# Kernel optimization log

Hardware: AMD Instinct MI355X
Metric: run time of the kernel (lower is better)

Reference implementation:

```python
import jax, jax.numpy as jnp
import numpy as np

B, S = 2, 256
CN, CE = 256, 128        # node / edge channels
A, H, V = 32, 8, 32      # attention_size, heads, value_size
AH, VH = A * H, V * H


def setup_inputs() -> dict:
    key = jax.random.key(0)
    ks = jax.random.split(key, 16)
    w = lambda k, shape: (jax.random.normal(k, shape) * 0.05).astype(jnp.float32)
    nodes = jax.random.normal(ks[0], (B, CN, S), dtype=jnp.float32)
    edges = jax.random.normal(ks[1], (B, CE, S, S), dtype=jnp.float32)
    lengths = jnp.array([S, (3 * S) // 4])            # padded-batch valid lengths
    mask = jnp.arange(S)[None, :] < lengths[:, None]  # (B, S) bool
    return dict(
        nodes=nodes, edges=edges, mask=mask,
        Wq=w(ks[2], (AH, CN)),
        Wk=w(ks[3], (AH, CN + CE)),
        Wv=w(ks[4], (VH, CN + CE)),
        Wo=w(ks[5], (CN, VH)),
        We=w(ks[6], (CE, VH + CE)),
        Wm1=w(ks[7], (CN, CN)), bm1=jnp.zeros((CN,), jnp.float32),
        Wm2=w(ks[8], (CN, CN)), bm2=jnp.zeros((CN,), jnp.float32),
        We1=w(ks[9], (CE, CE)), be1=jnp.zeros((CE,), jnp.float32),
        We2=w(ks[10], (CE, CE)), be2=jnp.zeros((CE,), jnp.float32),
        an0=(jax.random.normal(ks[11], (CN,)) * 0.1).astype(jnp.float32),
        an1=(jax.random.normal(ks[12], (CN,)) * 0.1).astype(jnp.float32),
        ae0=(jax.random.normal(ks[13], (CE,)) * 0.1).astype(jnp.float32),
        ae1=(jax.random.normal(ks[14], (CE,)) * 0.1).astype(jnp.float32),
    )


def _block(nodes, edges, mask, Wq, Wk, Wv, Wo, We,
           Wm1, bm1, Wm2, bm2, We1, be1, We2, be2, an0, an1, ae0, ae1):
    relu = jax.nn.relu
    b, _, s = nodes.shape
    # node MLP (1x1 conv, ReLU, 1x1 conv, ReLU) + ReZero residual; dropout in eval mode = identity
    h = relu(jnp.einsum('oc,bcs->bos', Wm1, nodes) + bm1[None, :, None])
    h = relu(jnp.einsum('oc,bcs->bos', Wm2, h) + bm2[None, :, None])
    nodes = nodes + an0[None, :, None] * h
    # edge MLP (1x1 conv2d) + ReZero residual
    g = relu(jnp.einsum('oc,bcij->boij', We1, edges) + be1[None, :, None, None])
    g = relu(jnp.einsum('oc,bcij->boij', We2, g) + be2[None, :, None, None])
    edges = edges + ae0[None, :, None, None] * g
    # materialized multi-head attention
    q = jnp.einsum('ac,bcs->bas', Wq, nodes).reshape(b, H, A, s)            # (B,H,A,S)
    ne = jnp.concatenate([jnp.broadcast_to(nodes[:, :, :, None], (b, CN, s, s)), edges], axis=1)
    k = jnp.einsum('ac,bcij->baij', Wk, ne).reshape(b, H, A, s, s)          # (B,H,A,S,S)
    v = jnp.einsum('vc,bcij->bvij', Wv, ne).reshape(b, H, V, s, s)          # (B,H,V,S,S)
    sim = jnp.einsum('bhai,bhaij->bhij', q, k) / jnp.sqrt(jnp.float32(A))   # (B,H,S,S)
    sim = jnp.where(mask[:, None, None, :], sim, jnp.float32(-1e9))
    sim = jax.nn.softmax(sim, axis=-1)
    mm = (mask[:, None, None, :] & mask[:, None, :, None]).astype(sim.dtype)  # (B,1,S,S)
    sim = sim * mm
    v = v * mm[:, None]
    nf = jnp.einsum('bhij,bhvij->bhvi', sim, v).reshape(b, H * V, s)        # (B,HV,S)
    node_att = jnp.einsum('oc,bcs->bos', Wo, nf)
    # edge features: broadcast node features along j, symmetrize via transpose+average
    ef = 0.5 * (nf[:, :, :, None] + nf[:, :, None, :])                      # (B,HV,S,S)
    edge_att = jnp.einsum('oc,bcij->boij', We, jnp.concatenate([ef, edges], axis=1))
    # ReZero residuals (project_* are Identity since in_size == out_size)
    nodes = nodes + an1[None, :, None] * node_att
    edges = edges + ae1[None, :, None, None] * edge_att
    # final masking
    nodes = nodes * mask[:, None, :].astype(nodes.dtype)
    edges = edges * mm
    return nodes, edges


def reference(nodes, edges, mask, Wq, Wk, Wv, Wo, We, Wm1, bm1, Wm2, bm2,
              We1, be1, We2, be2, an0, an1, ae0, ae1):
    return _block(nodes, edges, mask, Wq, Wk, Wv, Wo, We,
                  Wm1, bm1, Wm2, bm2, We1, be1, We2, be2, an0, an1, ae0, ae1)
```

## Files before the change

### kernel.cpp

```cpp
#include <hip/hip_runtime.h>
#include <hip/hip_bf16.h>
#include <cstdint>
#include <cstddef>

constexpr int B_  = 2;
constexpr int S_  = 256;
constexpr int CN_ = 256;
constexpr int CE_ = 128;
constexpr int A_  = 32;
constexpr int H_  = 8;
constexpr int V_  = 32;
constexpr int AH_ = A_ * H_;
constexpr int VH_ = V_ * H_;
constexpr int SS_ = S_ * S_;
constexpr int CNE_ = CN_ + CE_;

constexpr size_t OFF_N1   = 0;
constexpr size_t OFF_Q    = OFF_N1  + (size_t)B_*CN_*S_;
constexpr size_t OFF_VN   = OFF_Q   + (size_t)B_*AH_*S_;
constexpr size_t OFF_NF   = OFF_VN  + (size_t)B_*VH_*S_;
constexpr size_t OFF_WNF  = OFF_NF  + (size_t)B_*VH_*S_;
constexpr size_t OFF_WB1  = OFF_WNF + (size_t)B_*CE_*S_;
constexpr size_t OFF_WB2  = OFF_WB1 + 16384;
constexpr size_t OFF_WBE  = OFF_WB2 + 16384;
constexpr size_t OFF_WKT  = OFF_WBE + 16384;
constexpr size_t OFF_MASK = OFF_WKT + 32768;

__device__ inline uint16_t f2bf(float x) {
    uint32_t u = __float_as_uint(x);
    uint32_t r = (u + 0x7fffu + ((u >> 16) & 1u)) >> 16;
    return (uint16_t)r;
}
__device__ inline float bf2f(uint16_t h) {
    return __uint_as_float(((uint32_t)h) << 16);
}
__device__ inline uint32_t pack_split(float v) {
    uint32_t hi = (uint32_t)f2bf(v);
    float res = v - __uint_as_float(hi << 16);
    return (hi << 16) | (__float_as_uint(res) >> 16);
}
__device__ inline float unpack_f32(uint32_t p) {
    return __uint_as_float(p & 0xffff0000u) + __uint_as_float(p << 16);
}

typedef __attribute__((ext_vector_type(8))) short sh8;
typedef __attribute__((ext_vector_type(4))) short sh4;
typedef __attribute__((ext_vector_type(4))) float f32x4;

#define MFMA_B16(a, b, c) __builtin_amdgcn_mfma_f32_16x16x32_bf16((a), (b), (c), 0, 0, 0)

__device__ inline int eidx(int j, int c) {
    return (j * 136 + c) ^ (((j >> 3) & 7) << 3);
}

#define GEMM4_K256(WROW, XS, A0, A1, A2, A3)                                   \
    for (int c = 0; c < 256; c += 4) {                                         \
        float4 w  = *(const float4*)((WROW) + c);                              \
        float4 x0 = *(const float4*)((XS) + (c+0)*4);                          \
        float4 x1 = *(const float4*)((XS) + (c+1)*4);                          \
        float4 x2 = *(const float4*)((XS) + (c+2)*4);                          \
        float4 x3 = *(const float4*)((XS) + (c+3)*4);                          \
        A0 = fmaf(w.x,x0.x,fmaf(w.y,x1.x,fmaf(w.z,x2.x,fmaf(w.w,x3.x,A0))));   \
        A1 = fmaf(w.x,x0.y,fmaf(w.y,x1.y,fmaf(w.z,x2.y,fmaf(w.w,x3.y,A1))));   \
        A2 = fmaf(w.x,x0.z,fmaf(w.y,x1.z,fmaf(w.z,x2.z,fmaf(w.w,x3.z,A2))));   \
        A3 = fmaf(w.x,x0.w,fmaf(w.y,x1.w,fmaf(w.z,x2.w,fmaf(w.w,x3.w,A3))));   \
    }

__global__ void k_mask_norm(const unsigned char* __restrict__ mraw,
                            float* __restrict__ ws)
{
    int t = threadIdx.x;
    unsigned char b1 = mraw[1], b2 = mraw[2];
    float mv;
    if (b1 == (unsigned char)1) {
        mv = mraw[t] ? 1.f : 0.f;
    } else if (b2 == (unsigned char)128) {
        mv = (((const float*)mraw)[t] != 0.f) ? 1.f : 0.f;
    } else {
        mv = (((const int*)mraw)[t] != 0) ? 1.f : 0.f;
    }
    ws[OFF_MASK + t] = mv;
}

__global__ void k_wprep(const float* __restrict__ We1_,
                        const float* __restrict__ We2_,
                        const float* __restrict__ We_,
                        const float* __restrict__ Wk_,
                        float* __restrict__ ws)
{
    int idx = blockIdx.x * 256 + threadIdx.x;
    int m = idx >> 14;
    if (m < 3) {
        int r = idx & 16383;
        int o = r >> 7, c = r & 127;
        ushort* wb1 = (ushort*)(ws + OFF_WB1);
        ushort* wb2 = (ushort*)(ws + OFF_WB2);
        ushort* wbe = (ushort*)(ws + OFF_WBE);
        if (m == 0)      wb1[r] = f2bf(We1_[o*CE_ + c]);
        else if (m == 1) wb2[r] = f2bf(We2_[o*CE_ + c]);
        else             wbe[r] = f2bf(We_[o*CNE_ + CN_ + c]);
    } else {
        int r = idx - 49152;
        int a = r >> 10, h = (r >> 7) & 7, c = r & 127;
        ws[OFF_WKT + r] = Wk_[(size_t)(h*A_ + a)*CNE_ + CN_ + c];
    }
}

__global__ __launch_bounds__(256)
void k_node_mlp_qv(const float* __restrict__ nodes,
                   const float* __restrict__ Wm1, const float* __restrict__ bm1,
                   const float* __restrict__ Wm2, const float* __restrict__ bm2,
                   const float* __restrict__ an0,
                   const float* __restrict__ Wq,  const float* __restrict__ Wv,
                   float* __restrict__ ws)
{
    __shared__ float xs[CN_ * 4];
    __shared__ float hs[CN_ * 4];
    const int t  = threadIdx.x;
    const int b  = blockIdx.x >> 6;
    const int s0 = (blockIdx.x & 63) * 4;

    {
        float4 nv = *(const float4*)(nodes + (size_t)(b*CN_+t)*S_ + s0);
        xs[t*4+0]=nv.x; xs[t*4+1]=nv.y; xs[t*4+2]=nv.z; xs[t*4+3]=nv.w;
    }
    __syncthreads();

    float a0, a1, a2, a3;
    {
        float bv = bm1[t]; a0=bv; a1=bv; a2=bv; a3=bv;
        GEMM4_K256(Wm1 + t*CN_, xs, a0, a1, a2, a3);
        hs[t*4+0]=fmaxf(a0,0.f); hs[t*4+1]=fmaxf(a1,0.f);
        hs[t*4+2]=fmaxf(a2,0.f); hs[t*4+3]=fmaxf(a3,0.f);
    }
    __syncthreads();
    {
        float bv = bm2[t]; a0=bv; a1=bv; a2=bv; a3=bv;
        GEMM4_K256(Wm2 + t*CN_, hs, a0, a1, a2, a3);
    }
    {
        float an = an0[t];
        float n0 = xs[t*4+0] + an*fmaxf(a0,0.f);
        float n1 = xs[t*4+1] + an*fmaxf(a1,0.f);
        float n2 = xs[t*4+2] + an*fmaxf(a2,0.f);
        float n3 = xs[t*4+3] + an*fmaxf(a3,0.f);
        xs[t*4+0]=n0; xs[t*4+1]=n1; xs[t*4+2]=n2; xs[t*4+3]=n3;
        *(float4*)(ws + OFF_N1 + (size_t)(b*CN_+t)*S_ + s0) = make_float4(n0,n1,n2,n3);
    }
    __syncthreads();

    {
        a0=0.f; a1=0.f; a2=0.f; a3=0.f;
        GEMM4_K256(Wq + t*CN_, xs, a0, a1, a2, a3);
        const float rsA = 0.1767766952966369f;
        *(float4*)(ws + OFF_Q + (size_t)(b*AH_+t)*S_ + s0) =
            make_float4(a0*rsA, a1*rsA, a2*rsA, a3*rsA);
    }
    {
        a0=0.f; a1=0.f; a2=0.f; a3=0.f;
        GEMM4_K256(Wv + t*CNE_, xs, a0, a1, a2, a3);
        *(float4*)(ws + OFF_VN + (size_t)(b*VH_+t)*S_ + s0) = make_float4(a0,a1,a2,a3);
    }
}

__global__ __launch_bounds__(256, 2)
void k_edge_mlp(const float* __restrict__ edges,
                const float* __restrict__ ws,
                const float* __restrict__ be1, const float* __restrict__ be2,
                const float* __restrict__ ae0,
                uint32_t* __restrict__ e1out)
{
    __shared__ ushort Ehi[64 * 136];
    __shared__ ushort Elo[64 * 136];
    __shared__ ushort Ht [64 * 136];

    const int t  = threadIdx.x;
    const int b  = blockIdx.x >> 10;
    const int i  = (blockIdx.x >> 2) & 255;
    const int j0 = (blockIdx.x & 3) * 64;
    const float* Eb = edges + (size_t)b*CE_*SS_ + (size_t)i*S_ + j0;

    {
        const int tj = t & 15;
        const int p0 = t >> 4;
        #pragma unroll
        for (int s = 0; s < 4; ++s) {
            int c = (s*16 + p0) * 2;
            float4 v0 = *(const float4*)(Eb + (size_t)c*SS_ + tj*4);
            float4 v1 = *(const float4*)(Eb + (size_t)(c+1)*SS_ + tj*4);
            float q0[4] = {v0.x, v0.y, v0.z, v0.w};
            float q1[4] = {v1.x, v1.y, v1.z, v1.w};
            #pragma unroll
            for (int jj = 0; jj < 4; ++jj) {
                int j = tj*4 + jj;
                uint32_t h0 = (uint32_t)f2bf(q0[jj]);
                uint32_t h1 = (uint32_t)f2bf(q1[jj]);
                float r0 = q0[jj] - __uint_as_float(h0 << 16);
                float r1 = q1[jj] - __uint_as_float(h1 << 16);
                int us = eidx(j, c);
                *(uint32_t*)&Ehi[us] = h0 | (h1 << 16);
                *(uint32_t*)&Elo[us] = (__float_as_uint(r0) >> 16)
                                     | (__float_as_uint(r1) & 0xffff0000u);
            }
        }
    }

    const int w  = t >> 6;
    const int l  = t & 63;
    const int lr = l & 15;
    const int lk = l >> 4;
    const ushort* wb1 = (const ushort*)(ws + OFF_WB1);
    const ushort* wb2 = (const ushort*)(ws + OFF_WB2);
    sh8 A1[2][4], A2[2][4];
    #pragma unroll
    for (int mt = 0; mt < 2; ++mt) {
        int o = w*32 + mt*16 + lr;
        #pragma unroll
        for (int ks = 0; ks < 4; ++ks) {
            A1[mt][ks] = *(const sh8*)(wb1 + o*CE_ + ks*32 + lk*8);
            A2[mt][ks] = *(const sh8*)(wb2 + o*CE_ + ks*32 + lk*8);
        }
    }

    f32x4 acc1[2][4];
    #pragma unroll
    for (int mt = 0; mt < 2; ++mt) {
        float4 bv = *(const float4*)(be1 + w*32 + mt*16 + lk*4);
        #pragma unroll
        for (int nt = 0; nt < 4; ++nt) {
            acc1[mt][nt][0] = bv.x; acc1[mt][nt][1] = bv.y;
            acc1[mt][nt][2] = bv.z; acc1[mt][nt][3] = bv.w;
        }
    }
    __syncthreads();
    #pragma unroll
    for (int nt = 0; nt < 4; ++nt) {
        int j = nt*16 + lr;
        sh8 bh[4];
        #pragma unroll
        for (int ks = 0; ks < 4; ++ks)
            bh[ks] = *(const sh8*)&Ehi[eidx(j, ks*32 + lk*8)];
        #pragma unroll
        for (int mt = 0; mt < 2; ++mt)
            #pragma unroll
            for (int ks = 0; ks < 4; ++ks)
                acc1[mt][nt] = MFMA_B16(A1[mt][ks], bh[ks], acc1[mt][nt]);
    }

    #pragma unroll
    for (int mt = 0; mt < 2; ++mt)
        #pragma unroll
        for (int nt = 0; nt < 4; ++nt) {
            int o0 = w*32 + mt*16 + lk*4;
            int j  = nt*16 + lr;
            uint32_t u0 = __float_as_uint(fmaxf(acc1[mt][nt][0], 0.f));
            uint32_t u1 = __float_as_uint(fmaxf(acc1[mt][nt][1], 0.f));
            uint32_t u2 = __float_as_uint(fmaxf(acc1[mt][nt][2], 0.f));
            uint32_t u3 = __float_as_uint(fmaxf(acc1[mt][nt][3], 0.f));
            int us = eidx(j, o0);
            *(uint32_t*)&Ht[us]     = (u0 >> 16) | (u1 & 0xffff0000u);
            *(uint32_t*)&Ht[us + 2] = (u2 >> 16) | (u3 & 0xffff0000u);
        }
    __syncthreads();

    f32x4 acc2[2][4];
    #pragma unroll
    for (int mt = 0; mt < 2; ++mt) {
        float4 bv = *(const float4*)(be2 + w*32 + mt*16 + lk*4);
        #pragma unroll
        for (int nt = 0; nt < 4; ++nt) {
            acc2[mt][nt][0] = bv.x; acc2[mt][nt][1] = bv.y;
            acc2[mt][nt][2] = bv.z; acc2[mt][nt][3] = bv.w;
        }
    }
    #pragma unroll
    for (int nt = 0; nt < 4; ++nt) {
        int j = nt*16 + lr;
        sh8 hh[4];
        #pragma unroll
        for (int ks = 0; ks < 4; ++ks)
            hh[ks] = *(const sh8*)&Ht[eidx(j, ks*32 + lk*8)];
        #pragma unroll
        for (int mt = 0; mt < 2; ++mt)
            #pragma unroll
            for (int ks = 0; ks < 4; ++ks)
                acc2[mt][nt] = MFMA_B16(A2[mt][ks], hh[ks], acc2[mt][nt]);
    }

    #pragma unroll
    for (int mt = 0; mt < 2; ++mt) {
        int o0 = w*32 + mt*16 + lk*4;
        float4 a0v = *(const float4*)(ae0 + o0);
        float aev[4] = {a0v.x, a0v.y, a0v.z, a0v.w};
        #pragma unroll
        for (int nt = 0; nt < 4; ++nt) {
            int j = nt*16 + lr;
            int us = eidx(j, o0);
            sh4 eh = *(const sh4*)&Ehi[us];
            sh4 el = *(const sh4*)&Elo[us];
            #pragma unroll
            for (int r = 0; r < 4; ++r) {
                float e = bf2f((uint16_t)eh[r]) + bf2f((uint16_t)el[r]);
                float g = fmaxf(acc2[mt][nt][r], 0.f);
                e1out[(size_t)(b*CE_ + o0 + r)*SS_ + (size_t)i*S_ + j0 + j] =
                    pack_split(e + aev[r]*g);
            }
        }
    }
}

__global__ __launch_bounds__(256)
void k_attn(const uint32_t* __restrict__ e1, float* __restrict__ ws,
            const float* __restrict__ Wv)
{
    __shared__ float qcol[AH_];
    __shared__ float qw[CE_ * 8];
    __shared__ float simL[H_ * S_];
    __shared__ float Etile[CE_ * 65];
    __shared__ float seL[1024];
    const int t = threadIdx.x;
    const int b = blockIdx.x >> 8, i = blockIdx.x & 255;
    const float* maskf = ws + OFF_MASK;

    qcol[t] = ws[OFF_Q + (size_t)(b*AH_+t)*S_ + i];
    __syncthreads();

    {
        const float* WkT = ws + OFF_WKT;
        #pragma unroll
        for (int k = 0; k < 4; ++k) {
            int idx = k*256 + t;
            int c = idx & 127, h = idx >> 7;
            float acc = 0.f;
            #pragma unroll 8
            for (int aa = 0; aa < A_; ++aa)
                acc = fmaf(qcol[h*A_ + aa], WkT[aa*1024 + h*128 + c], acc);
            qw[c*8 + h] = acc;
        }
    }
    __syncthreads();

    const uint32_t* Eb = e1 + ((size_t)(b*CE_)*S_ + i)*S_;
    float sv[8];
    #pragma unroll
    for (int h = 0; h < 8; ++h) sv[h] = 0.f;
    for (int c = 0; c < CE_; ++c) {
        float e = unpack_f32(Eb[(size_t)c*SS_ + t]);
        float4 q0 = *(const float4*)(qw + c*8);
        float4 q1 = *(const float4*)(qw + c*8 + 4);
        sv[0] = fmaf(q0.x, e, sv[0]); sv[1] = fmaf(q0.y, e, sv[1]);
        sv[2] = fmaf(q0.z, e, sv[2]); sv[3] = fmaf(q0.w, e, sv[3]);
        sv[4] = fmaf(q1.x, e, sv[4]); sv[5] = fmaf(q1.y, e, sv[5]);
        sv[6] = fmaf(q1.z, e, sv[6]); sv[7] = fmaf(q1.w, e, sv[7]);
    }
    const bool mj = maskf[b*S_ + t] != 0.f;
    #pragma unroll
    for (int h = 0; h < 8; ++h) simL[h*S_ + t] = mj ? sv[h] : -1e9f;
    __syncthreads();

    {
        const int h = t >> 5, l = t & 31;
        float vv[8]; float m = -3.4e38f;
        #pragma unroll
        for (int k = 0; k < 8; ++k) { vv[k] = simL[h*S_ + l + k*32]; m = fmaxf(m, vv[k]); }
        #pragma unroll
        for (int off = 16; off >= 1; off >>= 1) m = fmaxf(m, __shfl_xor(m, off, 32));
        float ssum = 0.f; float ex[8];
        #pragma unroll
        for (int k = 0; k < 8; ++k) { ex[k] = __expf(vv[k] - m); ssum += ex[k]; }
        #pragma unroll
        for (int off = 16; off >= 1; off >>= 1) ssum += __shfl_xor(ssum, off, 32);
        const float mi = maskf[b*S_ + i];
        const float rr = mi / ssum;
        #pragma unroll
        for (int k = 0; k < 8; ++k) simL[h*S_ + l + k*32] = ex[k] * rr;
    }
    __syncthreads();

    const int cp = t & 127, hg = t >> 7;
    float a4[4] = {0.f, 0.f, 0.f, 0.f};
    for (int jt = 0; jt < 4; ++jt) {
        #pragma unroll 4
        for (int r = 0; r < 32; ++r) {
            int idx = r*256 + t;
            int c = idx >> 6, j = idx & 63;
            Etile[c*65 + j] = unpack_f32(Eb[(size_t)c*SS_ + jt*64 + j]);
        }
        __syncthreads();
        for (int j = 0; j < 64; ++j) {
            float e = Etile[cp*65 + j];
            #pragma unroll
            for (int k = 0; k < 4; ++k)
                a4[k] = fmaf(e, simL[(hg*4+k)*S_ + jt*64 + j], a4[k]);
        }
        __syncthreads();
    }
    #pragma unroll
    for (int k = 0; k < 4; ++k) seL[(hg*4+k)*128 + cp] = a4[k];
    __syncthreads();

    {
        const int h2 = t >> 5;
        float acc = 0.f;
        const float* wvr = Wv + (size_t)t*CNE_ + CN_;
        for (int c = 0; c < CE_; c += 4) {
            float4 wv4 = *(const float4*)(wvr + c);
            acc = fmaf(wv4.x, seL[h2*128 + c],     acc);
            acc = fmaf(wv4.y, seL[h2*128 + c + 1], acc);
            acc = fmaf(wv4.z, seL[h2*128 + c + 2], acc);
            acc = fmaf(wv4.w, seL[h2*128 + c + 3], acc);
        }
        const float mi = maskf[b*S_ + i];
        float nfv = ws[OFF_VN + (size_t)(b*VH_+t)*S_ + i] * mi + acc;
        ws[OFF_NF + (size_t)(b*VH_+t)*S_ + i] = nfv;
    }
}

__global__ __launch_bounds__(256)
void k_node_out(float* __restrict__ ws, const float* __restrict__ Wo,
                const float* __restrict__ We, const float* __restrict__ an1,
                float* __restrict__ out_nodes)
{
    __shared__ float xs[VH_ * 4];
    const int t  = threadIdx.x;
    const int b  = blockIdx.x >> 6;
    const int s0 = (blockIdx.x & 63) * 4;
    {
        float4 nv = *(const float4*)(ws + OFF_NF + (size_t)(b*VH_+t)*S_ + s0);
        xs[t*4+0]=nv.x; xs[t*4+1]=nv.y; xs[t*4+2]=nv.z; xs[t*4+3]=nv.w;
    }
    __syncthreads();
    float a0=0.f, a1=0.f, a2=0.f, a3=0.f;
    GEMM4_K256(Wo + t*VH_, xs, a0, a1, a2, a3);
    {
        float aw = an1[t];
        float4 n1 = *(const float4*)(ws + OFF_N1 + (size_t)(b*CN_+t)*S_ + s0);
        float4 mk = *(const float4*)(ws + OFF_MASK + b*S_ + s0);
        *(float4*)(out_nodes + (size_t)(b*CN_+t)*S_ + s0) = make_float4(
            (n1.x + aw*a0) * mk.x, (n1.y + aw*a1) * mk.y,
            (n1.z + aw*a2) * mk.z, (n1.w + aw*a3) * mk.w);
    }
    if (t < CE_) {
        a0=0.f; a1=0.f; a2=0.f; a3=0.f;
        GEMM4_K256(We + t*CNE_, xs, a0, a1, a2, a3);
        *(float4*)(ws + OFF_WNF + (size_t)(b*CE_+t)*S_ + s0) = make_float4(a0,a1,a2,a3);
    }
}

__global__ __launch_bounds__(256, 2)
void k_edge_out(const uint32_t* __restrict__ e1p, float* __restrict__ e1f,
                const float* __restrict__ ws, const float* __restrict__ ae1)
{
    __shared__ ushort Ehi[64 * 136];
    __shared__ ushort Elo[64 * 136];
    __shared__ float  wni_s[CE_];

    const int t  = threadIdx.x;
    const int b  = blockIdx.x >> 10;
    const int i  = (blockIdx.x >> 2) & 255;
    const int j0 = (blockIdx.x & 3) * 64;
    const uint32_t* Ebp = e1p + (size_t)b*CE_*SS_ + (size_t)i*S_ + j0;
    float*          Ebf = e1f + (size_t)b*CE_*SS_ + (size_t)i*S_ + j0;
    const float* Wnf   = ws + OFF_WNF;
    const float* maskf = ws + OFF_MASK;

    if (t < CE_) wni_s[t] = Wnf[(size_t)(b*CE_ + t)*S_ + i];

    {
        const int tj = t & 15;
        const int p0 = t >> 4;
        #pragma unroll
        for (int s = 0; s < 4; ++s) {
            int c = (s*16 + p0) * 2;
            uint4 v0 = *(const uint4*)(Ebp + (size_t)c*SS_ + tj*4);
            uint4 v1 = *(const uint4*)(Ebp + (size_t)(c+1)*SS_ + tj*4);
            uint32_t w0[4] = {v0.x, v0.y, v0.z, v0.w};
            uint32_t w1[4] = {v1.x, v1.y, v1.z, v1.w};
            #pragma unroll
            for (int jj = 0; jj < 4; ++jj) {
                int j = tj*4 + jj;
                int us = eidx(j, c);
                *(uint32_t*)&Ehi[us] = (w0[jj] >> 16) | (w1[jj] & 0xffff0000u);
                *(uint32_t*)&Elo[us] = (w0[jj] & 0xffffu) | (w1[jj] << 16);
            }
        }
    }

    const int w  = t >> 6;
    const int l  = t & 63;
    const int lr = l & 15;
    const int lk = l >> 4;
    const ushort* wbe = (const ushort*)(ws + OFF_WBE);
    sh8 AE[2][4];
    #pragma unroll
    for (int mt = 0; mt < 2; ++mt) {
        int o = w*32 + mt*16 + lr;
        #pragma unroll
        for (int ks = 0; ks < 4; ++ks)
            AE[mt][ks] = *(const sh8*)(wbe + o*CE_ + ks*32 + lk*8);
    }

    f32x4 acc[2][4];
    #pragma unroll
    for (int mt = 0; mt < 2; ++mt)
        #pragma unroll
        for (int nt = 0; nt < 4; ++nt)
            acc[mt][nt] = (f32x4){0.f, 0.f, 0.f, 0.f};
    __syncthreads();
    #pragma unroll
    for (int nt = 0; nt < 4; ++nt) {
        int j = nt*16 + lr;
        sh8 bh[4];
        #pragma unroll
        for (int ks = 0; ks < 4; ++ks)
            bh[ks] = *(const sh8*)&Ehi[eidx(j, ks*32 + lk*8)];
        #pragma unroll
        for (int mt = 0; mt < 2; ++mt)
            #pragma unroll
            for (int ks = 0; ks < 4; ++ks)
                acc[mt][nt] = MFMA_B16(AE[mt][ks], bh[ks], acc[mt][nt]);
    }

    const float mi = maskf[b*S_ + i];
    #pragma unroll
    for (int mt = 0; mt < 2; ++mt) {
        int o0 = w*32 + mt*16 + lk*4;
        float4 a1v = *(const float4*)(ae1 + o0);
        float aev[4] = {a1v.x, a1v.y, a1v.z, a1v.w};
        #pragma unroll
        for (int nt = 0; nt < 4; ++nt) {
            int j  = nt*16 + lr;
            int jg = j0 + j;
            float mjv = maskf[b*S_ + jg];
            int us = eidx(j, o0);
            sh4 eh = *(const sh4*)&Ehi[us];
            sh4 el = *(const sh4*)&Elo[us];
            #pragma unroll
            for (int r = 0; r < 4; ++r) {
                float e   = bf2f((uint16_t)eh[r]) + bf2f((uint16_t)el[r]);
                float att = 0.5f*(wni_s[o0+r] + Wnf[(size_t)(b*CE_+o0+r)*S_ + jg])
                          + acc[mt][nt][r];
                Ebf[(size_t)(o0+r)*SS_ + j] = (e + aev[r]*att) * (mi * mjv);
            }
        }
    }
}

extern "C" void kernel_launch(void* const* d_in, const int* in_sizes, int n_in,
                              void* d_out, int out_size, void* d_ws, size_t ws_size,
                              hipStream_t stream)
{
    const float* nodes = (const float*)d_in[0];
    const float* edges = (const float*)d_in[1];
    const unsigned char* mraw = (const unsigned char*)d_in[2];
    const float* Wq  = (const float*)d_in[3];
    const float* Wk  = (const float*)d_in[4];
    const float* Wv  = (const float*)d_in[5];
    const float* Wo  = (const float*)d_in[6];
    const float* We  = (const float*)d_in[7];
    const float* Wm1 = (const float*)d_in[8];
    const float* bm1 = (const float*)d_in[9];
    const float* Wm2 = (const float*)d_in[10];
    const float* bm2 = (const float*)d_in[11];
    const float* We1 = (const float*)d_in[12];
    const float* be1 = (const float*)d_in[13];
    const float* We2 = (const float*)d_in[14];
    const float* be2 = (const float*)d_in[15];
    const float* an0 = (const float*)d_in[16];
    const float* an1 = (const float*)d_in[17];
    const float* ae0 = (const float*)d_in[18];
    const float* ae1 = (const float*)d_in[19];

    float* ws = (float*)d_ws;
    float* out_nodes = (float*)d_out;
    float* out_edges = out_nodes + (size_t)B_*CN_*S_;

    k_mask_norm  <<<1,    512, 0, stream>>>(mraw, ws);
    k_wprep      <<<320,  256, 0, stream>>>(We1, We2, We, Wk, ws);
    k_node_mlp_qv<<<128,  256, 0, stream>>>(nodes, Wm1, bm1, Wm2, bm2, an0, Wq, Wv, ws);
    k_edge_mlp   <<<2048, 256, 0, stream>>>(edges, ws, be1, be2, ae0, (uint32_t*)out_edges);
    k_attn       <<<512,  256, 0, stream>>>((const uint32_t*)out_edges, ws, Wv);
    k_node_out   <<<128,  256, 0, stream>>>(ws, Wo, We, an1, out_nodes);
    k_edge_out   <<<2048, 256, 0, stream>>>((const uint32_t*)out_edges, out_edges, ws, ae1);
}
```

Measured before the change: 301.3 us.

## Fuse attention score and value passes with online softmax over shared edge tiles

The attention kernel used to read each block's edge row from global memory twice, once for the q·k scores and again for the value aggregation. It now loads each 64-column edge tile into shared memory once with 128-bit loads, computes partial scores from that tile, and updates an online softmax with running max and sum rescaling before accumulating the value sums. Wv is also pre-transposed in the weight-prep kernel, so the final projection reads it coalesced. In exchange the kernel needs more barriers per tile and more shared memory, which may lower occupancy.

```diff
diff --git a/kernel.cpp b/kernel.cpp
--- a/kernel.cpp
+++ b/kernel.cpp
@@ -24,7 +24,8 @@
 constexpr size_t OFF_WB2  = OFF_WB1 + 16384;
 constexpr size_t OFF_WBE  = OFF_WB2 + 16384;
 constexpr size_t OFF_WKT  = OFF_WBE + 16384;
-constexpr size_t OFF_MASK = OFF_WKT + 32768;
+constexpr size_t OFF_WVT  = OFF_WKT + 32768;
+constexpr size_t OFF_MASK = OFF_WVT + 32768;
 
 __device__ inline uint16_t f2bf(float x) {
     uint32_t u = __float_as_uint(x);
@@ -86,11 +87,12 @@
                         const float* __restrict__ We2_,
                         const float* __restrict__ We_,
                         const float* __restrict__ Wk_,
+                        const float* __restrict__ Wv_,
                         float* __restrict__ ws)
 {
     int idx = blockIdx.x * 256 + threadIdx.x;
-    int m = idx >> 14;
-    if (m < 3) {
+    if (idx < 49152) {
+        int m = idx >> 14;
         int r = idx & 16383;
         int o = r >> 7, c = r & 127;
         ushort* wb1 = (ushort*)(ws + OFF_WB1);
@@ -99,10 +101,14 @@
         if (m == 0)      wb1[r] = f2bf(We1_[o*CE_ + c]);
         else if (m == 1) wb2[r] = f2bf(We2_[o*CE_ + c]);
         else             wbe[r] = f2bf(We_[o*CNE_ + CN_ + c]);
-    } else {
+    } else if (idx < 81920) {
         int r = idx - 49152;
         int a = r >> 10, h = (r >> 7) & 7, c = r & 127;
         ws[OFF_WKT + r] = Wk_[(size_t)(h*A_ + a)*CNE_ + CN_ + c];
+    } else {
+        int r = idx - 81920;
+        int c = r >> 8, o = r & 255;
+        ws[OFF_WVT + r] = Wv_[(size_t)o*CNE_ + CN_ + c];
     }
 }
 
@@ -310,23 +316,31 @@
 }
 
 __global__ __launch_bounds__(256)
-void k_attn(const uint32_t* __restrict__ e1, float* __restrict__ ws,
-            const float* __restrict__ Wv)
-{
-    __shared__ float qcol[AH_];
+void k_attn(const uint32_t* __restrict__ e1, float* __restrict__ ws)
+{
+    __shared__ float Ef[128 * 67];
     __shared__ float qw[CE_ * 8];
-    __shared__ float simL[H_ * S_];
-    __shared__ float Etile[CE_ * 65];
-    __shared__ float seL[1024];
+    __shared__ float seA[8 * 128];
+    __shared__ float pL[8 * 64];
+    __shared__ float part[4 * 8 * 64];
+    __shared__ float mrow[8], srow[8], fh[8];
+    float* qcol = part;
+
     const int t = threadIdx.x;
     const int b = blockIdx.x >> 8, i = blockIdx.x & 255;
     const float* maskf = ws + OFF_MASK;
 
     qcol[t] = ws[OFF_Q + (size_t)(b*AH_+t)*S_ + i];
+    {
+        #pragma unroll
+        for (int r = 0; r < 4; ++r) seA[r*256 + t] = 0.f;
+        if (t < 8) { mrow[t] = -3.4e38f; srow[t] = 0.f; fh[t] = 0.f; }
+    }
     __syncthreads();
 
     {
         const float* WkT = ws + OFF_WKT;
+        float q[4];
         #pragma unroll
         for (int k = 0; k < 4; ++k) {
             int idx = k*256 + t;
@@ -335,83 +349,111 @@
             #pragma unroll 8
             for (int aa = 0; aa < A_; ++aa)
                 acc = fmaf(qcol[h*A_ + aa], WkT[aa*1024 + h*128 + c], acc);
-            qw[c*8 + h] = acc;
-        }
-    }
-    __syncthreads();
-
-    const uint32_t* Eb = e1 + ((size_t)(b*CE_)*S_ + i)*S_;
-    float sv[8];
-    #pragma unroll
-    for (int h = 0; h < 8; ++h) sv[h] = 0.f;
-    for (int c = 0; c < CE_; ++c) {
-        float e = unpack_f32(Eb[(size_t)c*SS_ + t]);
-        float4 q0 = *(const float4*)(qw + c*8);
-        float4 q1 = *(const float4*)(qw + c*8 + 4);
-        sv[0] = fmaf(q0.x, e, sv[0]); sv[1] = fmaf(q0.y, e, sv[1]);
-        sv[2] = fmaf(q0.z, e, sv[2]); sv[3] = fmaf(q0.w, e, sv[3]);
-        sv[4] = fmaf(q1.x, e, sv[4]); sv[5] = fmaf(q1.y, e, sv[5]);
-        sv[6] = fmaf(q1.z, e, sv[6]); sv[7] = fmaf(q1.w, e, sv[7]);
-    }
-    const bool mj = maskf[b*S_ + t] != 0.f;
-    #pragma unroll
-    for (int h = 0; h < 8; ++h) simL[h*S_ + t] = mj ? sv[h] : -1e9f;
-    __syncthreads();
-
-    {
-        const int h = t >> 5, l = t & 31;
-        float vv[8]; float m = -3.4e38f;
-        #pragma unroll
-        for (int k = 0; k < 8; ++k) { vv[k] = simL[h*S_ + l + k*32]; m = fmaxf(m, vv[k]); }
-        #pragma unroll
-        for (int off = 16; off >= 1; off >>= 1) m = fmaxf(m, __shfl_xor(m, off, 32));
-        float ssum = 0.f; float ex[8];
-        #pragma unroll
-        for (int k = 0; k < 8; ++k) { ex[k] = __expf(vv[k] - m); ssum += ex[k]; }
-        #pragma unroll
-        for (int off = 16; off >= 1; off >>= 1) ssum += __shfl_xor(ssum, off, 32);
+            q[k] = acc;
+        }
+        __syncthreads();
+        #pragma unroll
+        for (int k = 0; k < 4; ++k) {
+            int idx = k*256 + t;
+            int c = idx & 127, h = idx >> 7;
+            qw[c*8 + h] = q[k];
+        }
+    }
+    __syncthreads();
+
+    const uint32_t* Ebp = e1 + ((size_t)(b*CE_)*S_ + i)*S_;
+    const int tj = t & 15;
+    const int tc = t >> 4;
+    const int jj = t & 63;
+    const int cc = t >> 6;
+
+    for (int jt = 0; jt < 4; ++jt) {
+        #pragma unroll
+        for (int s = 0; s < 8; ++s) {
+            int c = s*16 + tc;
+            uint4 v = *(const uint4*)(Ebp + (size_t)c*SS_ + jt*64 + tj*4);
+            Ef[c*67 + tj*4 + 0] = unpack_f32(v.x);
+            Ef[c*67 + tj*4 + 1] = unpack_f32(v.y);
+            Ef[c*67 + tj*4 + 2] = unpack_f32(v.z);
+            Ef[c*67 + tj*4 + 3] = unpack_f32(v.w);
+        }
+        __syncthreads();
+
+        {
+            float s0=0,s1=0,s2=0,s3=0,s4=0,s5=0,s6=0,s7=0;
+            for (int k = 0; k < 32; ++k) {
+                int c = cc*32 + k;
+                float e = Ef[c*67 + jj];
+                float4 q0 = *(const float4*)(qw + c*8);
+                float4 q1 = *(const float4*)(qw + c*8 + 4);
+                s0 = fmaf(q0.x, e, s0); s1 = fmaf(q0.y, e, s1);
+                s2 = fmaf(q0.z, e, s2); s3 = fmaf(q0.w, e, s3);
+                s4 = fmaf(q1.x, e, s4); s5 = fmaf(q1.y, e, s5);
+                s6 = fmaf(q1.z, e, s6); s7 = fmaf(q1.w, e, s7);
+            }
+            float* pp = part + cc*512 + jj;
+            pp[0*64]=s0; pp[1*64]=s1; pp[2*64]=s2; pp[3*64]=s3;
+            pp[4*64]=s4; pp[5*64]=s5; pp[6*64]=s6; pp[7*64]=s7;
+        }
+        __syncthreads();
+
+        #pragma unroll
+        for (int r = 0; r < 2; ++r) {
+            int idx = r*256 + t;
+            int h = idx >> 6, j = idx & 63;
+            float sim = part[h*64 + j] + part[512 + h*64 + j]
+                      + part[1024 + h*64 + j] + part[1536 + h*64 + j];
+            float mj = maskf[b*S_ + jt*64 + j];
+            pL[h*64 + j] = (mj != 0.f) ? sim : -1e9f;
+        }
+        __syncthreads();
+
+        {
+            const int h = t >> 5, l = t & 31;
+            float v0 = pL[h*64 + l], v1 = pL[h*64 + l + 32];
+            float tm = fmaxf(v0, v1);
+            #pragma unroll
+            for (int off = 16; off >= 1; off >>= 1) tm = fmaxf(tm, __shfl_xor(tm, off, 32));
+            float mold = mrow[h];
+            float mnew = fmaxf(mold, tm);
+            float e0 = __expf(v0 - mnew), e1v = __expf(v1 - mnew);
+            float ts = e0 + e1v;
+            #pragma unroll
+            for (int off = 16; off >= 1; off >>= 1) ts += __shfl_xor(ts, off, 32);
+            pL[h*64 + l] = e0; pL[h*64 + l + 32] = e1v;
+            if (l == 0) {
+                float f = __expf(mold - mnew);
+                srow[h] = srow[h]*f + ts;
+                mrow[h] = mnew;
+                fh[h] = f;
+            }
+        }
+        __syncthreads();
+
+        #pragma unroll
+        for (int r = 0; r < 4; ++r) {
+            int idx = r*256 + t;
+            int h = idx >> 7, cp = idx & 127;
+            float acc = seA[idx] * fh[h];
+            const float* er = Ef + cp*67;
+            const float* pr = pL + h*64;
+            #pragma unroll 8
+            for (int j = 0; j < 64; ++j)
+                acc = fmaf(pr[j], er[j], acc);
+            seA[idx] = acc;
+        }
+        __syncthreads();
+    }
+
+    {
+        const int h2 = t >> 5;
+        const float* WvT = ws + OFF_WVT;
+        float acc = 0.f;
+        for (int c = 0; c < CE_; ++c)
+            acc = fmaf(WvT[c*256 + t], seA[h2*128 + c], acc);
         const float mi = maskf[b*S_ + i];
-        const float rr = mi / ssum;
-        #pragma unroll
-        for (int k = 0; k < 8; ++k) simL[h*S_ + l + k*32] = ex[k] * rr;
-    }
-    __syncthreads();
-
-    const int cp = t & 127, hg = t >> 7;
-    float a4[4] = {0.f, 0.f, 0.f, 0.f};
-    for (int jt = 0; jt < 4; ++jt) {
-        #pragma unroll 4
-        for (int r = 0; r < 32; ++r) {
-            int idx = r*256 + t;
-            int c = idx >> 6, j = idx & 63;
-            Etile[c*65 + j] = unpack_f32(Eb[(size_t)c*SS_ + jt*64 + j]);
-        }
-        __syncthreads();
-        for (int j = 0; j < 64; ++j) {
-            float e = Etile[cp*65 + j];
-            #pragma unroll
-            for (int k = 0; k < 4; ++k)
-                a4[k] = fmaf(e, simL[(hg*4+k)*S_ + jt*64 + j], a4[k]);
-        }
-        __syncthreads();
-    }
-    #pragma unroll
-    for (int k = 0; k < 4; ++k) seL[(hg*4+k)*128 + cp] = a4[k];
-    __syncthreads();
-
-    {
-        const int h2 = t >> 5;
-        float acc = 0.f;
-        const float* wvr = Wv + (size_t)t*CNE_ + CN_;
-        for (int c = 0; c < CE_; c += 4) {
-            float4 wv4 = *(const float4*)(wvr + c);
-            acc = fmaf(wv4.x, seL[h2*128 + c],     acc);
-            acc = fmaf(wv4.y, seL[h2*128 + c + 1], acc);
-            acc = fmaf(wv4.z, seL[h2*128 + c + 2], acc);
-            acc = fmaf(wv4.w, seL[h2*128 + c + 3], acc);
-        }
-        const float mi = maskf[b*S_ + i];
-        float nfv = ws[OFF_VN + (size_t)(b*VH_+t)*S_ + i] * mi + acc;
+        float nfv = ws[OFF_VN + (size_t)(b*VH_+t)*S_ + i] * mi
+                  + acc * (mi / srow[h2]);
         ws[OFF_NF + (size_t)(b*VH_+t)*S_ + i] = nfv;
     }
 }
@@ -576,10 +618,10 @@
     float* out_edges = out_nodes + (size_t)B_*CN_*S_;
 
     k_mask_norm  <<<1,    512, 0, stream>>>(mraw, ws);
-    k_wprep      <<<320,  256, 0, stream>>>(We1, We2, We, Wk, ws);
+    k_wprep      <<<448,  256, 0, stream>>>(We1, We2, We, Wk, Wv, ws);
     k_node_mlp_qv<<<128,  256, 0, stream>>>(nodes, Wm1, bm1, Wm2, bm2, an0, Wq, Wv, ws);
     k_edge_mlp   <<<2048, 256, 0, stream>>>(edges, ws, be1, be2, ae0, (uint32_t*)out_edges);
-    k_attn       <<<512,  256, 0, stream>>>((const uint32_t*)out_edges, ws, Wv);
+    k_attn       <<<512,  256, 0, stream>>>((const uint32_t*)out_edges, ws);
     k_node_out   <<<128,  256, 0, stream>>>(ws, Wo, We, an1, out_nodes);
     k_edge_out   <<<2048, 256, 0, stream>>>((const uint32_t*)out_edges, out_edges, ws, ae1);
 }
```

Result: faster. 292.2 us (-3.0%).
